# Performance work log

Hardware: AMD Instinct MI355X
Metric: run time of the kernel (lower is better)

Reference implementation:

```python
import jax, jax.numpy as jnp
import numpy as np

N = 8192
EMB = 256
NHID = 64
ALPHA = 0.2  # LeakyReLU negative slope
NEG_INF = -9e15


def setup_inputs() -> dict:
    key = jax.random.key(0)
    k1, k2, k3, k4 = jax.random.split(key, 4)
    inp = jax.random.normal(k1, (N, EMB), dtype=jnp.float32)
    adj = jax.random.randint(k2, (N, N), 0, 2, dtype=jnp.int32)
    W = jax.random.normal(k3, (EMB, NHID), dtype=jnp.float32) * 0.05
    a = jax.random.normal(k4, (2 * NHID,), dtype=jnp.float32) * 0.05
    return {"input": inp, "adj": adj, "W": W, "a": a}


def reference(input, adj, W, a):
    # h = W(input): [N, nhid]
    h = input @ W
    # e_ij = leakyrelu(h_i . a[:nhid] + h_j . a[nhid:])  (equiv. to concat-pairs @ a)
    s_src = h @ a[:NHID]   # [N]
    s_dst = h @ a[NHID:]   # [N]
    e = jax.nn.leaky_relu(s_src[:, None] + s_dst[None, :], ALPHA)  # [N, N]
    attention = jnp.where(adj > 0, e, NEG_INF)
    attention = jax.nn.softmax(attention, axis=1)
    # edge dropout p=0.0 (eval) -> identity
    h_prime = attention @ h  # [N, nhid]
    return h_prime
```

## Files before the change

### kernel.cpp

```cpp
#include <hip/hip_runtime.h>
#include <hip/hip_bf16.h>

#define N_NODES 8192
#define EMB 256
#define NHID 64
#define LOG2E 1.44269504088896340736f
#define S_SPLIT 32
#define COLS 256
#define NKT 8
#define HROW 264
#define MROW 36

typedef __attribute__((ext_vector_type(8))) short bf16x8;
typedef __attribute__((ext_vector_type(4))) float f32x4;

static __device__ __forceinline__ short f2bf(float f) {
  __hip_bfloat16 h = __float2bfloat16(f);
  return *reinterpret_cast<short*>(&h);
}

static __device__ __forceinline__ short f2bf_fast(float f) {
  unsigned u = __builtin_bit_cast(unsigned, f);
  return (short)((u + 0x8000u) >> 16);
}

__global__ __launch_bounds__(256) void gat_k1(
    const float* __restrict__ in, const float* __restrict__ W,
    const float* __restrict__ a, short* __restrict__ hT,
    float* __restrict__ ssrc, float* __restrict__ sdst) {
  int wave = threadIdx.x >> 6, lane = threadIdx.x & 63;
  int row = blockIdx.x * 4 + wave;
  int d = lane;
  const float4* in4 = reinterpret_cast<const float4*>(in + (size_t)row * EMB);
  float acc = 0.f;
#pragma unroll 4
  for (int k4 = 0; k4 < EMB / 4; ++k4) {
    float4 x = in4[k4];
    int k = k4 * 4;
    acc = fmaf(x.x, W[(k + 0) * NHID + d], acc);
    acc = fmaf(x.y, W[(k + 1) * NHID + d], acc);
    acc = fmaf(x.z, W[(k + 2) * NHID + d], acc);
    acc = fmaf(x.w, W[(k + 3) * NHID + d], acc);
  }
  hT[(size_t)d * N_NODES + row] = f2bf(acc);
  float p1 = acc * a[d];
  float p2 = acc * a[NHID + d];
#pragma unroll
  for (int off = 32; off > 0; off >>= 1) {
    p1 += __shfl_xor(p1, off);
    p2 += __shfl_xor(p2, off);
  }
  if (lane == 0) {
    ssrc[row] = p1 * LOG2E;
    sdst[row] = p2 * LOG2E;
  }
}

__global__ __launch_bounds__(256, 4) void gat_k2(
    const int* __restrict__ adj, const short* __restrict__ hT,
    const float* __restrict__ ssrc, const float* __restrict__ sdst,
    float* __restrict__ pacc, float* __restrict__ pz) {
  __shared__ short hlds[64 * HROW];
  __shared__ unsigned char mlds[64 * MROW];
  __shared__ float tlds[COLS];

  int split = blockIdx.x >> 7;
  int rb = blockIdx.x & 127;
  int tid = threadIdx.x;
  int c0 = split * COLS;
  int wv = tid >> 6, lane = tid & 63;

#pragma unroll
  for (int p = 0; p < 8; ++p) {
    int flat = p * 4096 + tid * 16;
    int srow = flat >> 9;
    int scol = (flat & 511) >> 1;
    bf16x8 v = *reinterpret_cast<const bf16x8*>(
        hT + (size_t)srow * N_NODES + c0 + scol);
    *reinterpret_cast<bf16x8*>(&hlds[srow * HROW + scol]) = v;
  }
  if (tid < 64) {
    float4 t4 = *reinterpret_cast<const float4*>(sdst + c0 + tid * 4);
    *reinterpret_cast<float4*>(&tlds[tid * 4]) = t4;
  }
  {
    int h = lane >> 5, sl = lane & 31;
#pragma unroll
    for (int p = 0; p < 8; ++p) {
      int r = wv * 16 + p * 2 + h;
      const int* ap = adj + (size_t)(rb * 64 + r) * N_NODES + c0 + sl * 8;
      int4 v0 = *reinterpret_cast<const int4*>(ap);
      int4 v1 = *reinterpret_cast<const int4*>(ap + 4);
      unsigned b = (unsigned)(v0.x != 0) | ((unsigned)(v0.y != 0) << 1) |
                   ((unsigned)(v0.z != 0) << 2) | ((unsigned)(v0.w != 0) << 3) |
                   ((unsigned)(v1.x != 0) << 4) | ((unsigned)(v1.y != 0) << 5) |
                   ((unsigned)(v1.z != 0) << 6) | ((unsigned)(v1.w != 0) << 7);
      mlds[r * MROW + sl] = (unsigned char)b;
    }
  }
  __syncthreads();

  int lrow = lane & 15, kg = lane >> 4;
  int r0 = rb * 64 + wv * 16;
  float s_i = ssrc[r0 + lrow];

  f32x4 acc0 = {0.f, 0.f, 0.f, 0.f};
  f32x4 acc1 = acc0, acc2 = acc0, acc3 = acc0;
  float zacc = 0.f;

#pragma unroll
  for (int kt = 0; kt < NKT; ++kt) {
    int cb = kt * 32 + kg * 8;
    unsigned mb = mlds[(wv * 16 + lrow) * MROW + kt * 4 + kg];
    float4 tA = *reinterpret_cast<const float4*>(&tlds[cb]);
    float4 tB = *reinterpret_cast<const float4*>(&tlds[cb + 4]);
    bf16x8 b0 = *reinterpret_cast<const bf16x8*>(&hlds[(lrow + 0) * HROW + cb]);
    bf16x8 b1 = *reinterpret_cast<const bf16x8*>(&hlds[(lrow + 16) * HROW + cb]);
    bf16x8 b2 = *reinterpret_cast<const bf16x8*>(&hlds[(lrow + 32) * HROW + cb]);
    bf16x8 b3 = *reinterpret_cast<const bf16x8*>(&hlds[(lrow + 48) * HROW + cb]);

    float tv[8] = {tA.x, tA.y, tA.z, tA.w, tB.x, tB.y, tB.z, tB.w};
    bf16x8 af;
#pragma unroll
    for (int e = 0; e < 8; ++e) {
      float x = s_i + tv[e];
      float lk = fmaxf(x, 0.2f * x);
      float ev = __builtin_amdgcn_exp2f(lk);
      float w = (mb & (1u << e)) ? ev : 0.f;
      zacc += w;
      af[e] = f2bf_fast(w);
    }
    acc0 = __builtin_amdgcn_mfma_f32_16x16x32_bf16(af, b0, acc0, 0, 0, 0);
    acc1 = __builtin_amdgcn_mfma_f32_16x16x32_bf16(af, b1, acc1, 0, 0, 0);
    acc2 = __builtin_amdgcn_mfma_f32_16x16x32_bf16(af, b2, acc2, 0, 0, 0);
    acc3 = __builtin_amdgcn_mfma_f32_16x16x32_bf16(af, b3, acc3, 0, 0, 0);
  }

  float z = zacc;
  z += __shfl_xor(z, 16);
  z += __shfl_xor(z, 32);
  if (lane < 16) pz[(size_t)split * N_NODES + r0 + lane] = z;

  float* pa = pacc + (size_t)split * (N_NODES * NHID);
#pragma unroll
  for (int reg = 0; reg < 4; ++reg) {
    int orow = r0 + kg * 4 + reg;
    pa[(size_t)orow * NHID + 0 * 16 + lrow] = acc0[reg];
    pa[(size_t)orow * NHID + 1 * 16 + lrow] = acc1[reg];
    pa[(size_t)orow * NHID + 2 * 16 + lrow] = acc2[reg];
    pa[(size_t)orow * NHID + 3 * 16 + lrow] = acc3[reg];
  }
}

__global__ __launch_bounds__(256) void gat_k3(
    const float* __restrict__ pacc, const float* __restrict__ pz,
    float* __restrict__ out) {
  int t = blockIdx.x * 256 + threadIdx.x;
  int row = t >> 4;
  float4 num = {0.f, 0.f, 0.f, 0.f};
  float den = 0.f;
#pragma unroll 8
  for (int s = 0; s < S_SPLIT; ++s) {
    float4 p = *reinterpret_cast<const float4*>(
        &pacc[(size_t)s * (N_NODES * NHID) + (size_t)t * 4]);
    num.x += p.x; num.y += p.y; num.z += p.z; num.w += p.w;
    den += pz[(size_t)s * N_NODES + row];
  }
  float r = 1.f / den;
  float4 o = {num.x * r, num.y * r, num.z * r, num.w * r};
  *reinterpret_cast<float4*>(&out[(size_t)t * 4]) = o;
}

extern "C" void kernel_launch(void* const* d_in, const int* in_sizes, int n_in,
                              void* d_out, int out_size, void* d_ws, size_t ws_size,
                              hipStream_t stream) {
  (void)in_sizes; (void)n_in; (void)out_size; (void)ws_size;
  const float* in = (const float*)d_in[0];
  const int* adj = (const int*)d_in[1];
  const float* W = (const float*)d_in[2];
  const float* a = (const float*)d_in[3];
  float* out = (float*)d_out;

  char* w = (char*)d_ws;
  short* hT = (short*)w;
  float* ssrc = (float*)(w + (1u << 20));
  float* sdst = ssrc + N_NODES;
  float* pz = sdst + N_NODES;
  float* pacc = pz + (size_t)S_SPLIT * N_NODES;

  gat_k1<<<N_NODES / 4, 256, 0, stream>>>(in, W, a, hT, ssrc, sdst);
  gat_k2<<<128 * S_SPLIT, 256, 0, stream>>>(adj, hT, ssrc, sdst, pacc, pz);
  gat_k3<<<(N_NODES * NHID) / (256 * 4), 256, 0, stream>>>(pacc, pz, out);
}
```

Measured before the change: 419.1 us.

## Pre-pack adjacency into bitmask in fused first kernel, read bitmask in attention kernel

Adds a packing stage, merged into the projection kernel as extra blocks, that turns the int32 adjacency matrix into a 64-bit-per-group bitmask using wave ballots. The attention kernel then loads compact mask bytes instead of reading and comparing full int32 adjacency tiles. This moves the mask construction off the MFMA kernel's critical path. In exchange, the 256 MB adjacency read still happens once, and it adds a workspace write and read of the 8 MB mask plus an extra pass ordering dependency.

```diff
diff --git a/kernel.cpp b/kernel.cpp
--- a/kernel.cpp
+++ b/kernel.cpp
@@ -9,7 +9,9 @@
 #define COLS 256
 #define NKT 8
 #define HROW 264
-#define MROW 36
+#define MROW 40
+#define PACK_BLOCKS 2048
+#define K1_BLOCKS 2048
 
 typedef __attribute__((ext_vector_type(8))) short bf16x8;
 typedef __attribute__((ext_vector_type(4))) float f32x4;
@@ -24,12 +26,24 @@
   return (short)((u + 0x8000u) >> 16);
 }
 
-__global__ __launch_bounds__(256) void gat_k1(
+__global__ __launch_bounds__(256) void gat_k01(
+    const int* __restrict__ adj, unsigned long long* __restrict__ mask64,
     const float* __restrict__ in, const float* __restrict__ W,
     const float* __restrict__ a, short* __restrict__ hT,
     float* __restrict__ ssrc, float* __restrict__ sdst) {
-  int wave = threadIdx.x >> 6, lane = threadIdx.x & 63;
-  int row = blockIdx.x * 4 + wave;
+  int wv = threadIdx.x >> 6, lane = threadIdx.x & 63;
+  if (blockIdx.x < PACK_BLOCKS) {
+    const int NW = PACK_BLOCKS * 4;
+    const int NG = (N_NODES * N_NODES) / 64;
+    int wid = blockIdx.x * 4 + wv;
+    for (int g = wid; g < NG; g += NW) {
+      int v = adj[(size_t)g * 64 + lane];
+      unsigned long long bal = __ballot(v != 0);
+      if (lane == 0) mask64[g] = bal;
+    }
+    return;
+  }
+  int row = (blockIdx.x - PACK_BLOCKS) * 4 + wv;
   int d = lane;
   const float4* in4 = reinterpret_cast<const float4*>(in + (size_t)row * EMB);
   float acc = 0.f;
@@ -57,11 +71,11 @@
 }
 
 __global__ __launch_bounds__(256, 4) void gat_k2(
-    const int* __restrict__ adj, const short* __restrict__ hT,
+    const unsigned char* __restrict__ maskb, const short* __restrict__ hT,
     const float* __restrict__ ssrc, const float* __restrict__ sdst,
     float* __restrict__ pacc, float* __restrict__ pz) {
   __shared__ short hlds[64 * HROW];
-  __shared__ unsigned char mlds[64 * MROW];
+  __shared__ unsigned char mlds[64 * MROW] __attribute__((aligned(8)));
   __shared__ float tlds[COLS];
 
   int split = blockIdx.x >> 7;
@@ -84,19 +98,10 @@
     *reinterpret_cast<float4*>(&tlds[tid * 4]) = t4;
   }
   {
-    int h = lane >> 5, sl = lane & 31;
-#pragma unroll
-    for (int p = 0; p < 8; ++p) {
-      int r = wv * 16 + p * 2 + h;
-      const int* ap = adj + (size_t)(rb * 64 + r) * N_NODES + c0 + sl * 8;
-      int4 v0 = *reinterpret_cast<const int4*>(ap);
-      int4 v1 = *reinterpret_cast<const int4*>(ap + 4);
-      unsigned b = (unsigned)(v0.x != 0) | ((unsigned)(v0.y != 0) << 1) |
-                   ((unsigned)(v0.z != 0) << 2) | ((unsigned)(v0.w != 0) << 3) |
-                   ((unsigned)(v1.x != 0) << 4) | ((unsigned)(v1.y != 0) << 5) |
-                   ((unsigned)(v1.z != 0) << 6) | ((unsigned)(v1.w != 0) << 7);
-      mlds[r * MROW + sl] = (unsigned char)b;
-    }
+    int r = tid >> 2, k = tid & 3;
+    unsigned long long m = *reinterpret_cast<const unsigned long long*>(
+        maskb + (size_t)(rb * 64 + r) * (N_NODES / 8) + split * 32 + k * 8);
+    *reinterpret_cast<unsigned long long*>(&mlds[r * MROW + k * 8]) = m;
   }
   __syncthreads();
 
@@ -187,8 +192,12 @@
   float* sdst = ssrc + N_NODES;
   float* pz = sdst + N_NODES;
   float* pacc = pz + (size_t)S_SPLIT * N_NODES;
-
-  gat_k1<<<N_NODES / 4, 256, 0, stream>>>(in, W, a, hT, ssrc, sdst);
-  gat_k2<<<128 * S_SPLIT, 256, 0, stream>>>(adj, hT, ssrc, sdst, pacc, pz);
+  unsigned long long* mask64 =
+      (unsigned long long*)(pacc + (size_t)S_SPLIT * (N_NODES * NHID));
+
+  gat_k01<<<PACK_BLOCKS + K1_BLOCKS, 256, 0, stream>>>(adj, mask64, in, W, a,
+                                                       hT, ssrc, sdst);
+  gat_k2<<<128 * S_SPLIT, 256, 0, stream>>>((const unsigned char*)mask64, hT,
+                                            ssrc, sdst, pacc, pz);
   gat_k3<<<(N_NODES * NHID) / (256 * 4), 256, 0, stream>>>(pacc, pz, out);
 }
```

Result: slower. 449.3 us (+7.2%).

## Make gat_k2 persistent over row blocks with register-prefetched adjacency tiles

Applied to the files above, without the earlier changes.

Each block now handles NT=4 consecutive 64-row blocks for one column split. The hT slice it stages in LDS is reused across those row blocks instead of being reloaded per block. The next row block's adjacency ints are loaded into registers while the current block's exp/MFMA work runs, then packed into a double-buffered bitmask in LDS. This is meant to hide adjacency load latency and cut redundant hT staging. The cost is 4x fewer blocks (1024) and 64 extra VGPRs for the prefetch buffer, which may hurt occupancy under launch_bounds(256,4).

```diff
diff --git a/kernel.cpp b/kernel.cpp
--- a/kernel.cpp
+++ b/kernel.cpp
@@ -8,6 +8,7 @@
 #define S_SPLIT 32
 #define COLS 256
 #define NKT 8
+#define NT 4
 #define HROW 264
 #define MROW 36
 
@@ -56,20 +57,51 @@
   }
 }
 
+static __device__ __forceinline__ void adj_issue(
+    const int* __restrict__ adj, int rb, int c0, int wv, int lane,
+    int4 (&pre)[16]) {
+  int h = lane >> 5, sl = lane & 31;
+#pragma unroll
+  for (int p = 0; p < 8; ++p) {
+    int r = wv * 16 + p * 2 + h;
+    const int* ap = adj + (size_t)(rb * 64 + r) * N_NODES + c0 + sl * 8;
+    pre[p * 2 + 0] = *reinterpret_cast<const int4*>(ap);
+    pre[p * 2 + 1] = *reinterpret_cast<const int4*>(ap + 4);
+  }
+}
+
+static __device__ __forceinline__ void adj_pack(
+    const int4 (&pre)[16], unsigned char* __restrict__ mbuf, int wv, int lane) {
+  int h = lane >> 5, sl = lane & 31;
+#pragma unroll
+  for (int p = 0; p < 8; ++p) {
+    int r = wv * 16 + p * 2 + h;
+    int4 v0 = pre[p * 2 + 0], v1 = pre[p * 2 + 1];
+    unsigned b = (unsigned)(v0.x != 0) | ((unsigned)(v0.y != 0) << 1) |
+                 ((unsigned)(v0.z != 0) << 2) | ((unsigned)(v0.w != 0) << 3) |
+                 ((unsigned)(v1.x != 0) << 4) | ((unsigned)(v1.y != 0) << 5) |
+                 ((unsigned)(v1.z != 0) << 6) | ((unsigned)(v1.w != 0) << 7);
+    mbuf[r * MROW + sl] = (unsigned char)b;
+  }
+}
+
 __global__ __launch_bounds__(256, 4) void gat_k2(
     const int* __restrict__ adj, const short* __restrict__ hT,
     const float* __restrict__ ssrc, const float* __restrict__ sdst,
     float* __restrict__ pacc, float* __restrict__ pz) {
   __shared__ short hlds[64 * HROW];
-  __shared__ unsigned char mlds[64 * MROW];
+  __shared__ unsigned char mlds[2][64 * MROW];
   __shared__ float tlds[COLS];
 
-  int split = blockIdx.x >> 7;
-  int rb = blockIdx.x & 127;
+  int split = blockIdx.x & 31;
+  int slot = blockIdx.x >> 5;
   int tid = threadIdx.x;
   int c0 = split * COLS;
   int wv = tid >> 6, lane = tid & 63;
-
+  int lrow = lane & 15, kg = lane >> 4;
+
+  int4 pre[16];
+  adj_issue(adj, slot * NT, c0, wv, lane, pre);
 #pragma unroll
   for (int p = 0; p < 8; ++p) {
     int flat = p * 4096 + tid * 16;
@@ -83,72 +115,66 @@
     float4 t4 = *reinterpret_cast<const float4*>(sdst + c0 + tid * 4);
     *reinterpret_cast<float4*>(&tlds[tid * 4]) = t4;
   }
-  {
-    int h = lane >> 5, sl = lane & 31;
-#pragma unroll
-    for (int p = 0; p < 8; ++p) {
-      int r = wv * 16 + p * 2 + h;
-      const int* ap = adj + (size_t)(rb * 64 + r) * N_NODES + c0 + sl * 8;
-      int4 v0 = *reinterpret_cast<const int4*>(ap);
-      int4 v1 = *reinterpret_cast<const int4*>(ap + 4);
-      unsigned b = (unsigned)(v0.x != 0) | ((unsigned)(v0.y != 0) << 1) |
-                   ((unsigned)(v0.z != 0) << 2) | ((unsigned)(v0.w != 0) << 3) |
-                   ((unsigned)(v1.x != 0) << 4) | ((unsigned)(v1.y != 0) << 5) |
-                   ((unsigned)(v1.z != 0) << 6) | ((unsigned)(v1.w != 0) << 7);
-      mlds[r * MROW + sl] = (unsigned char)b;
+  adj_pack(pre, mlds[0], wv, lane);
+  __syncthreads();
+
+  float* pa = pacc + (size_t)split * (N_NODES * NHID);
+
+#pragma unroll
+  for (int t = 0; t < NT; ++t) {
+    int rb = slot * NT + t;
+    int cur = t & 1;
+    if (t + 1 < NT) adj_issue(adj, rb + 1, c0, wv, lane, pre);
+
+    int r0 = rb * 64 + wv * 16;
+    float s_i = ssrc[r0 + lrow];
+    f32x4 acc0 = {0.f, 0.f, 0.f, 0.f};
+    f32x4 acc1 = acc0, acc2 = acc0, acc3 = acc0;
+    float zacc = 0.f;
+
+#pragma unroll
+    for (int kt = 0; kt < NKT; ++kt) {
+      int cb = kt * 32 + kg * 8;
+      unsigned mb = mlds[cur][(wv * 16 + lrow) * MROW + kt * 4 + kg];
+      float4 tA = *reinterpret_cast<const float4*>(&tlds[cb]);
+      float4 tB = *reinterpret_cast<const float4*>(&tlds[cb + 4]);
+      bf16x8 b0 = *reinterpret_cast<const bf16x8*>(&hlds[(lrow + 0) * HROW + cb]);
+      bf16x8 b1 = *reinterpret_cast<const bf16x8*>(&hlds[(lrow + 16) * HROW + cb]);
+      bf16x8 b2 = *reinterpret_cast<const bf16x8*>(&hlds[(lrow + 32) * HROW + cb]);
+      bf16x8 b3 = *reinterpret_cast<const bf16x8*>(&hlds[(lrow + 48) * HROW + cb]);
+
+      float tv[8] = {tA.x, tA.y, tA.z, tA.w, tB.x, tB.y, tB.z, tB.w};
+      bf16x8 af;
+#pragma unroll
+      for (int e = 0; e < 8; ++e) {
+        float x = s_i + tv[e];
+        float lk = fmaxf(x, 0.2f * x);
+        float ev = __builtin_amdgcn_exp2f(lk);
+        float w = (mb & (1u << e)) ? ev : 0.f;
+        zacc += w;
+        af[e] = f2bf_fast(w);
+      }
+      acc0 = __builtin_amdgcn_mfma_f32_16x16x32_bf16(af, b0, acc0, 0, 0, 0);
+      acc1 = __builtin_amdgcn_mfma_f32_16x16x32_bf16(af, b1, acc1, 0, 0, 0);
+      acc2 = __builtin_amdgcn_mfma_f32_16x16x32_bf16(af, b2, acc2, 0, 0, 0);
+      acc3 = __builtin_amdgcn_mfma_f32_16x16x32_bf16(af, b3, acc3, 0, 0, 0);
     }
-  }
-  __syncthreads();
-
-  int lrow = lane & 15, kg = lane >> 4;
-  int r0 = rb * 64 + wv * 16;
-  float s_i = ssrc[r0 + lrow];
-
-  f32x4 acc0 = {0.f, 0.f, 0.f, 0.f};
-  f32x4 acc1 = acc0, acc2 = acc0, acc3 = acc0;
-  float zacc = 0.f;
-
-#pragma unroll
-  for (int kt = 0; kt < NKT; ++kt) {
-    int cb = kt * 32 + kg * 8;
-    unsigned mb = mlds[(wv * 16 + lrow) * MROW + kt * 4 + kg];
-    float4 tA = *reinterpret_cast<const float4*>(&tlds[cb]);
-    float4 tB = *reinterpret_cast<const float4*>(&tlds[cb + 4]);
-    bf16x8 b0 = *reinterpret_cast<const bf16x8*>(&hlds[(lrow + 0) * HROW + cb]);
-    bf16x8 b1 = *reinterpret_cast<const bf16x8*>(&hlds[(lrow + 16) * HROW + cb]);
-    bf16x8 b2 = *reinterpret_cast<const bf16x8*>(&hlds[(lrow + 32) * HROW + cb]);
-    bf16x8 b3 = *reinterpret_cast<const bf16x8*>(&hlds[(lrow + 48) * HROW + cb]);
-
-    float tv[8] = {tA.x, tA.y, tA.z, tA.w, tB.x, tB.y, tB.z, tB.w};
-    bf16x8 af;
-#pragma unroll
-    for (int e = 0; e < 8; ++e) {
-      float x = s_i + tv[e];
-      float lk = fmaxf(x, 0.2f * x);
-      float ev = __builtin_amdgcn_exp2f(lk);
-      float w = (mb & (1u << e)) ? ev : 0.f;
-      zacc += w;
-      af[e] = f2bf_fast(w);
+
+    float z = zacc;
+    z += __shfl_xor(z, 16);
+    z += __shfl_xor(z, 32);
+    if (lane < 16) pz[(size_t)split * N_NODES + r0 + lane] = z;
+#pragma unroll
+    for (int reg = 0; reg < 4; ++reg) {
+      int orow = r0 + kg * 4 + reg;
+      pa[(size_t)orow * NHID + 0 * 16 + lrow] = acc0[reg];
+      pa[(size_t)orow * NHID + 1 * 16 + lrow] = acc1[reg];
+      pa[(size_t)orow * NHID + 2 * 16 + lrow] = acc2[reg];
+      pa[(size_t)orow * NHID + 3 * 16 + lrow] = acc3[reg];
     }
-    acc0 = __builtin_amdgcn_mfma_f32_16x16x32_bf16(af, b0, acc0, 0, 0, 0);
-    acc1 = __builtin_amdgcn_mfma_f32_16x16x32_bf16(af, b1, acc1, 0, 0, 0);
-    acc2 = __builtin_amdgcn_mfma_f32_16x16x32_bf16(af, b2, acc2, 0, 0, 0);
-    acc3 = __builtin_amdgcn_mfma_f32_16x16x32_bf16(af, b3, acc3, 0, 0, 0);
-  }
-
-  float z = zacc;
-  z += __shfl_xor(z, 16);
-  z += __shfl_xor(z, 32);
-  if (lane < 16) pz[(size_t)split * N_NODES + r0 + lane] = z;
-
-  float* pa = pacc + (size_t)split * (N_NODES * NHID);
-#pragma unroll
-  for (int reg = 0; reg < 4; ++reg) {
-    int orow = r0 + kg * 4 + reg;
-    pa[(size_t)orow * NHID + 0 * 16 + lrow] = acc0[reg];
-    pa[(size_t)orow * NHID + 1 * 16 + lrow] = acc1[reg];
-    pa[(size_t)orow * NHID + 2 * 16 + lrow] = acc2[reg];
-    pa[(size_t)orow * NHID + 3 * 16 + lrow] = acc3[reg];
+
+    if (t + 1 < NT) adj_pack(pre, mlds[cur ^ 1], wv, lane);
+    __syncthreads();
   }
 }
 
@@ -189,6 +215,7 @@
   float* pacc = pz + (size_t)S_SPLIT * N_NODES;
 
   gat_k1<<<N_NODES / 4, 256, 0, stream>>>(in, W, a, hT, ssrc, sdst);
-  gat_k2<<<128 * S_SPLIT, 256, 0, stream>>>(adj, hT, ssrc, sdst, pacc, pz);
+  gat_k2<<<(128 / NT) * S_SPLIT, 256, 0, stream>>>(adj, hT, ssrc, sdst, pacc,
+                                                   pz);
   gat_k3<<<(N_NODES * NHID) / (256 * 4), 256, 0, stream>>>(pacc, pz, out);
 }
```

After: 425.5 us. Within noise of the previous version (+1.5%).
